# Optimization experiments

Hardware: AMD Instinct MI355X
Metric: run time of the kernel (lower is better)

Reference implementation:

```python
import math
import jax
import jax.numpy as jnp
import numpy as np
from jax import lax

HEADS = 4
TOPK = 8


def _gelu(x):
    return jax.nn.gelu(x, approximate=False)


def _ln(x, g, b, eps=1e-5):
    m = x.mean(-1, keepdims=True)
    v = ((x - m) ** 2).mean(-1, keepdims=True)
    return (x - m) * lax.rsqrt(v + eps) * g + b


def setup_inputs() -> dict:
    key = jax.random.key(0)
    ks = jax.random.split(key, 16)
    B, T, N, C, A = 16, 16, 196, 768, 192

    def w(k, shape, s=0.02):
        return jax.random.normal(k, shape, jnp.float32) * s

    return dict(
        x=w(ks[0], (B, T, N + 1, C), 1.0),
        down_w=w(ks[1], (A, C)), down_b=jnp.zeros((A,), jnp.float32),
        ldw_w=w(ks[2], (A, 1, 3, 3), 0.1),
        lpw_w=w(ks[3], (A, A), 0.05),
        lnorm_g=jnp.ones((A,), jnp.float32), lnorm_b=jnp.zeros((A,), jnp.float32),
        tdw_w=w(ks[4], (A, 1, 3), 0.1),
        tpw_w=w(ks[5], (A, A), 0.05),
        tmlp_w1=w(ks[6], (2 * A, A), 0.05), tmlp_b1=jnp.zeros((2 * A,), jnp.float32),
        tmlp_w2=w(ks[7], (A, 2 * A), 0.05), tmlp_b2=jnp.zeros((A,), jnp.float32),
        tnorm_g=jnp.ones((A,), jnp.float32), tnorm_b=jnp.zeros((A,), jnp.float32),
        attn_in_w=w(ks[8], (3 * A, A), 0.05), attn_in_b=jnp.zeros((3 * A,), jnp.float32),
        attn_out_w=w(ks[9], (A, A), 0.05), attn_out_b=jnp.zeros((A,), jnp.float32),
        aproj_w=w(ks[10], (A, A), 0.05), aproj_b=jnp.zeros((A,), jnp.float32),
        anorm_g=jnp.ones((A,), jnp.float32), anorm_b=jnp.zeros((A,), jnp.float32),
        gate_w1=w(ks[11], (A, 2 * A), 0.05), gate_b1=jnp.zeros((A,), jnp.float32),
        gate_w2=w(ks[12], (3 * A, A), 0.05), gate_b2=jnp.zeros((3 * A,), jnp.float32),
        up_w=w(ks[13], (C, A), 0.02), up_b=jnp.zeros((C,), jnp.float32),
        cls_w=w(ks[14], (C, A), 0.02), cls_b=jnp.zeros((C,), jnp.float32),
    )


def reference(x, down_w, down_b, ldw_w, lpw_w, lnorm_g, lnorm_b, tdw_w, tpw_w,
              tmlp_w1, tmlp_b1, tmlp_w2, tmlp_b2, tnorm_g, tnorm_b,
              attn_in_w, attn_in_b, attn_out_w, attn_out_b, aproj_w, aproj_b,
              anorm_g, anorm_b, gate_w1, gate_b1, gate_w2, gate_b2,
              up_w, up_b, cls_w, cls_b):
    cls_tok = x[:, :, :1, :]
    patch = x[:, :, 1:, :]
    b, t, n, _ = patch.shape
    hw = int(math.isqrt(n))
    a = down_w.shape[0]

    # down projection: [b,t,n,C] -> [b,t,n,A]
    ph = jnp.einsum('btnc,ac->btna', patch, down_w) + down_b
    # temporal difference, delta[:,0]=0
    delta = jnp.concatenate([jnp.zeros_like(ph[:, :1]), ph[:, 1:] - ph[:, :-1]], axis=1)

    # --- local path: depthwise 3x3 -> GELU -> pointwise 1x1 -> LN ---
    loc = ph.reshape(b * t, hw, hw, a).transpose(0, 3, 1, 2)  # (bt) a h w
    loc = lax.conv_general_dilated(loc, ldw_w, (1, 1), 'SAME',
                                   feature_group_count=a,
                                   dimension_numbers=('NCHW', 'OIHW', 'NCHW'))
    loc = _gelu(loc)
    loc = jnp.einsum('bchw,dc->bdhw', loc, lpw_w)
    loc = loc.transpose(0, 2, 3, 1).reshape(b, t, n, a)
    local = _ln(loc, lnorm_g, lnorm_b)

    # --- transition path: depthwise temporal conv -> GELU -> pointwise -> MLP -> LN ---
    tr = delta.transpose(0, 2, 3, 1).reshape(b * n, a, t)  # (bn) a t
    tr = lax.conv_general_dilated(tr, tdw_w, (1,), 'SAME',
                                  feature_group_count=a,
                                  dimension_numbers=('NCH', 'OIH', 'NCH'))
    tr = _gelu(tr)
    tr = jnp.einsum('nct,dc->ndt', tr, tpw_w)
    tr = tr.reshape(b, n, a, t).transpose(0, 3, 1, 2)  # b t n a
    h1 = _gelu(jnp.einsum('btna,ha->btnh', tr, tmlp_w1) + tmlp_b1)
    tr = jnp.einsum('btnh,ah->btna', h1, tmlp_w2) + tmlp_b2
    transition = _ln(tr, tnorm_g, tnorm_b)

    # --- relation anchor path: topk gather -> temporal MHA -> scatter_add -> LN ---
    kk = min(TOPK, n)
    sal = jnp.abs(delta).mean(-1)  # b t n
    _, idx = lax.top_k(sal, kk)    # b t k
    bi = jnp.arange(b)[:, None, None]
    ti = jnp.arange(t)[None, :, None]
    anchor = (ph + delta)[bi, ti, idx]  # b t k a
    tok = anchor.transpose(0, 2, 1, 3).reshape(b * kk, t, a)  # (bk) t a
    qkv = tok @ attn_in_w.T + attn_in_b
    q, k_, v = jnp.split(qkv, 3, axis=-1)
    dh = a // HEADS

    def heads(z):
        return z.reshape(b * kk, t, HEADS, dh).transpose(0, 2, 1, 3)

    q, k_, v = heads(q), heads(k_), heads(v)
    att = jax.nn.softmax(jnp.einsum('bhqd,bhkd->bhqk', q, k_) / math.sqrt(dh), axis=-1)
    out = jnp.einsum('bhqk,bhkd->bhqd', att, v).transpose(0, 2, 1, 3).reshape(b * kk, t, a)
    out = out @ attn_out_w.T + attn_out_b
    out = out @ aproj_w.T + aproj_b
    anchor_tok = out.reshape(b, kk, t, a).transpose(0, 2, 1, 3)  # b t k a
    anchor_map = jnp.zeros_like(ph).at[bi, ti, idx].add(anchor_tok)
    anchor_map = _ln(anchor_map, anorm_g, anorm_b)

    # --- softmax-gated 3-way fusion ---
    dp = jnp.abs(delta).mean((1, 2))      # b a
    ap = anchor_tok.mean((1, 2))          # b a
    g = jnp.concatenate([dp, ap], axis=-1)
    g = _gelu(g @ gate_w1.T + gate_b1) @ gate_w2.T + gate_b2
    gw = jax.nn.softmax(g.reshape(b, 3, a), axis=1)[:, :, None, None, :]
    fused = gw[:, 0] * local + gw[:, 1] * transition + gw[:, 2] * anchor_map

    patch_out = patch + fused @ up_w.T + up_b
    cls_out = cls_tok + fused.mean(2, keepdims=True) @ cls_w.T + cls_b
    return jnp.concatenate([cls_out, patch_out], axis=2)
```

## Files before the change

### kernel.cpp

```cpp
#include <hip/hip_runtime.h>
#include <math.h>

constexpr int Bb  = 16;
constexpr int Tt  = 16;
constexpr int Nn  = 196;
constexpr int Cc  = 768;
constexpr int Aa  = 192;
constexpr int KK  = 8;
constexpr int NCAND = 16;
constexpr int BT  = Bb * Tt;
constexpr int BTN = BT * Nn;
constexpr int BKT = Bb * KK * Tt;
constexpr size_t SZ = (size_t)BTN * Aa;

typedef unsigned short ushortt;
typedef __attribute__((ext_vector_type(8))) short bf16x8;
typedef __attribute__((ext_vector_type(4))) float f32x4;
typedef __attribute__((ext_vector_type(4))) unsigned short u16x4;
typedef __attribute__((ext_vector_type(8))) unsigned short u16x8;

static __device__ __forceinline__ float gelu_f(float x) {
  return 0.5f * x * (1.0f + erff(x * 0.7071067811865476f));
}
static __device__ __forceinline__ ushortt f2bf(float f) {
  unsigned u = __float_as_uint(f);
  u += 0x7FFFu + ((u >> 16) & 1u);
  return (ushortt)(u >> 16);
}
static __device__ __forceinline__ float bf2f(ushortt u) {
  return __uint_as_float(((unsigned)u) << 16);
}

template <typename AT, typename CT, int ROWMAP, int BIAS, int EPI>
__global__ __launch_bounds__(256) void gemm_mfma(
    const AT* __restrict__ Ain, const float* __restrict__ W,
    const float* __restrict__ bias, CT* __restrict__ Cout,
    const float* __restrict__ resid, int M, int Nc, int K) {
  constexpr int PIT = 40;
  __shared__ ushortt As[2][128 * PIT];
  __shared__ ushortt Bs[2][64 * PIT];
  const int tid = threadIdx.x;

  const int ncb = gridDim.x;
  const int nwg = ncb * gridDim.y;
  const int bid = blockIdx.y * ncb + blockIdx.x;
  const int cpx = nwg >> 3;
  const int swz = (bid & 7) * cpx + (bid >> 3);
  const int row0 = (swz / ncb) * 128;
  const int col0 = (swz % ncb) * 64;

  const int wid = tid >> 6;
  const int lane = tid & 63;
  const int wr = wid >> 1;
  const int wc = wid & 1;
  const int l15 = lane & 15;
  const int kgrp = lane >> 4;

  const int nsteps = K >> 5;

  const float* arowf[4];
  const ushortt* arowb[2];
  if constexpr (sizeof(AT) == 4) {
    const int quad = tid & 7, srow = tid >> 3;
#pragma unroll
    for (int p = 0; p < 4; ++p) {
      int r = row0 + srow + 32 * p;
      if (ROWMAP) {
        int bt = r / Nn;
        int n = r - bt * Nn;
        arowf[p] = (const float*)Ain + (size_t)(bt * (Nn + 1) + 1 + n) * K;
      } else {
        arowf[p] = (const float*)Ain + (size_t)r * K;
      }
    }
    (void)quad;
  } else {
    const int srow2 = tid >> 2;
#pragma unroll
    for (int p = 0; p < 2; ++p)
      arowb[p] = (const ushortt*)Ain + (size_t)(row0 + srow2 + 64 * p) * K;
  }
  const float* browp[2];
  {
    const int srow = tid >> 3;
#pragma unroll
    for (int p = 0; p < 2; ++p)
      browp[p] = W + (size_t)(col0 + srow + 32 * p) * K;
  }

  f32x4 acc[4][2];
#pragma unroll
  for (int i = 0; i < 4; ++i)
#pragma unroll
    for (int j = 0; j < 2; ++j) acc[i][j] = (f32x4){0.f, 0.f, 0.f, 0.f};

  float4 apre[4], bpre[2];
  u16x8 apreb[2];

#define STAGE_LOAD(k0)                                                       \
  if constexpr (sizeof(AT) == 4) {                                           \
    const int quad = tid & 7;                                                \
    _Pragma("unroll") for (int p = 0; p < 4; ++p)                            \
        apre[p] = *(const float4*)(arowf[p] + (k0) + quad * 4);              \
  } else {                                                                   \
    const int quad2 = tid & 3;                                               \
    _Pragma("unroll") for (int p = 0; p < 2; ++p)                            \
        apreb[p] = *(const u16x8*)(arowb[p] + (k0) + quad2 * 8);             \
  }                                                                          \
  {                                                                          \
    const int quad = tid & 7;                                                \
    _Pragma("unroll") for (int p = 0; p < 2; ++p)                            \
        bpre[p] = *(const float4*)(browp[p] + (k0) + quad * 4);              \
  }

#define STAGE_WRITE(buf)                                                     \
  if constexpr (sizeof(AT) == 4) {                                           \
    const int quad = tid & 7, srow = tid >> 3;                               \
    _Pragma("unroll") for (int p = 0; p < 4; ++p) {                          \
      u16x4 b = {f2bf(apre[p].x), f2bf(apre[p].y), f2bf(apre[p].z),          \
                 f2bf(apre[p].w)};                                           \
      *(u16x4*)&As[buf][(srow + 32 * p) * PIT + quad * 4] = b;               \
    }                                                                        \
  } else {                                                                   \
    const int quad2 = tid & 3, srow2 = tid >> 2;                             \
    _Pragma("unroll") for (int p = 0; p < 2; ++p)                            \
        *(u16x8*)&As[buf][(srow2 + 64 * p) * PIT + quad2 * 8] = apreb[p];    \
  }                                                                          \
  {                                                                          \
    const int quad = tid & 7, srow = tid >> 3;                               \
    _Pragma("unroll") for (int p = 0; p < 2; ++p) {                          \
      u16x4 b = {f2bf(bpre[p].x), f2bf(bpre[p].y), f2bf(bpre[p].z),          \
                 f2bf(bpre[p].w)};                                           \
      *(u16x4*)&Bs[buf][(srow + 32 * p) * PIT + quad * 4] = b;               \
    }                                                                        \
  }

  STAGE_LOAD(0);
  STAGE_WRITE(0);
  __syncthreads();

  int cur = 0;
  for (int step = 0; step < nsteps; ++step) {
    const bool pref = (step + 1 < nsteps);
    if (pref) {
      int k0 = (step + 1) << 5;
      STAGE_LOAD(k0);
    }
    bf16x8 af[4], bfv[2];
#pragma unroll
    for (int fm = 0; fm < 4; ++fm)
      af[fm] = *(const bf16x8*)&As[cur][(wr * 64 + fm * 16 + l15) * PIT + kgrp * 8];
#pragma unroll
    for (int fn = 0; fn < 2; ++fn)
      bfv[fn] = *(const bf16x8*)&Bs[cur][(wc * 32 + fn * 16 + l15) * PIT + kgrp * 8];
#pragma unroll
    for (int fm = 0; fm < 4; ++fm)
#pragma unroll
      for (int fn = 0; fn < 2; ++fn)
        acc[fm][fn] = __builtin_amdgcn_mfma_f32_16x16x32_bf16(
            af[fm], bfv[fn], acc[fm][fn], 0, 0, 0);
    if (pref) {
      STAGE_WRITE(cur ^ 1);
    }
    __syncthreads();
    cur ^= 1;
  }
#undef STAGE_LOAD
#undef STAGE_WRITE

#pragma unroll
  for (int fm = 0; fm < 4; ++fm) {
    int rbase = row0 + wr * 64 + fm * 16 + kgrp * 4;
#pragma unroll
    for (int fn = 0; fn < 2; ++fn) {
      int c = col0 + wc * 32 + fn * 16 + l15;
      float bv = BIAS ? bias[c] : 0.f;
#pragma unroll
      for (int j = 0; j < 4; ++j) {
        int r = rbase + j;
        float v = acc[fm][fn][j] + bv;
        if (EPI == 1) v = gelu_f(v);
        if (EPI == 2) {
          int bt = r / Nn;
          int n = r - bt * Nn;
          size_t off = (size_t)(bt * (Nn + 1) + 1 + n) * Nc + c;
          ((float*)Cout)[off] = resid[off] + v;
        } else {
          if constexpr (sizeof(CT) == 4)
            Cout[(size_t)r * Nc + c] = (CT)v;
          else
            ((ushortt*)Cout)[(size_t)r * Nc + c] = f2bf(v);
        }
      }
    }
  }
}

__global__ void delta_kernel(const float* __restrict__ ph,
                             float* __restrict__ delta,
                             float* __restrict__ dppart) {
  int bt = blockIdx.x;
  int t = bt & 15;
  int a = threadIdx.x;
  const float* cur = ph + (size_t)bt * Nn * Aa + a;
  float* dl = delta + (size_t)bt * Nn * Aa + a;
  float acc = 0.f;
  if (t == 0) {
    for (int n = 0; n < Nn; ++n) dl[(size_t)n * Aa] = 0.f;
  } else {
    const float* prev = cur - (size_t)Nn * Aa;
    for (int n = 0; n < Nn; ++n) {
      float d = cur[(size_t)n * Aa] - prev[(size_t)n * Aa];
      dl[(size_t)n * Aa] = d;
      acc += fabsf(d);
    }
  }
  dppart[bt * Aa + a] = acc;
}

__global__ void sal_kernel(const float* __restrict__ delta,
                           float* __restrict__ sal) {
  int row = blockIdx.x * 4 + (threadIdx.x >> 6);
  int lane = threadIdx.x & 63;
  const float* d = delta + (size_t)row * Aa;
  float s = fabsf(d[lane]) + fabsf(d[lane + 64]) + fabsf(d[lane + 128]);
#pragma unroll
  for (int off = 32; off > 0; off >>= 1) s += __shfl_xor(s, off, 64);
  if (lane == 0) sal[row] = s * (1.0f / 192.0f);
}

__global__ void topcand_kernel(const float* __restrict__ sal,
                               int* __restrict__ cand) {
  int bt = blockIdx.x;
  int lane = threadIdx.x;
  unsigned long long key[4];
#pragma unroll
  for (int j = 0; j < 4; ++j) {
    int n = lane + 64 * j;
    if (n < Nn) {
      unsigned fb = __float_as_uint(sal[(size_t)bt * Nn + n]);
      key[j] = ((unsigned long long)fb << 32) |
               (unsigned long long)(0xFFFFFFFFu - (unsigned)n);
    } else {
      key[j] = 0ULL;
    }
  }
  for (int r = 0; r < NCAND; ++r) {
    unsigned long long m = key[0];
    if (key[1] > m) m = key[1];
    if (key[2] > m) m = key[2];
    if (key[3] > m) m = key[3];
#pragma unroll
    for (int off = 32; off > 0; off >>= 1) {
      unsigned long long o = __shfl_xor(m, off, 64);
      if (o > m) m = o;
    }
    if (lane == 0)
      cand[bt * NCAND + r] = (int)(0xFFFFFFFFu - (unsigned)(m & 0xFFFFFFFFull));
#pragma unroll
    for (int j = 0; j < 4; ++j)
      if (key[j] == m) key[j] = 0ULL;
  }
}

__global__ __launch_bounds__(192) void refine_kernel(
    const float* __restrict__ x, const float* __restrict__ down_w,
    const int* __restrict__ cand, double* __restrict__ sal64) {
  int bt = blockIdx.x;
  int grp = blockIdx.y;
  int t = bt & 15;
  int a = threadIdx.x;
  if (t == 0) {
    if (a < 8) sal64[bt * NCAND + grp * 8 + a] = 0.0;
    return;
  }
  __shared__ double sdiff[8][Cc];
  __shared__ double sabs[8][Aa];
  const float* xt = x + (size_t)bt * (Nn + 1) * Cc;
  const float* xp = xt - (size_t)(Nn + 1) * Cc;
  for (int g = 0; g < 8; ++g) {
    int n = cand[bt * NCAND + grp * 8 + g];
    const float* rt = xt + (size_t)(1 + n) * Cc;
    const float* rp = xp + (size_t)(1 + n) * Cc;
    for (int c = a; c < Cc; c += 192)
      sdiff[g][c] = (double)rt[c] - (double)rp[c];
  }
  __syncthreads();
  double acc[8] = {};
  const float* wrow = down_w + (size_t)a * Cc;
  for (int c0 = 0; c0 < Cc; c0 += 4) {
    float4 w4 = *(const float4*)(wrow + c0);
#pragma unroll
    for (int g = 0; g < 8; ++g) {
      acc[g] += (double)w4.x * sdiff[g][c0] + (double)w4.y * sdiff[g][c0 + 1] +
                (double)w4.z * sdiff[g][c0 + 2] +
                (double)w4.w * sdiff[g][c0 + 3];
    }
  }
#pragma unroll
  for (int g = 0; g < 8; ++g) sabs[g][a] = fabs(acc[g]);
  __syncthreads();
  if (a < 8) {
    double s = 0.0;
    for (int i = 0; i < Aa; ++i) s += sabs[a][i];
    sal64[bt * NCAND + grp * 8 + a] = s * (1.0 / 192.0);
  }
}

__global__ void select_kernel(const double* __restrict__ sal64,
                              const int* __restrict__ cand,
                              int* __restrict__ idx) {
  int bt = blockIdx.x;
  int t = bt & 15;
  if (threadIdx.x != 0) return;
  if (t == 0) {
    for (int r = 0; r < KK; ++r) idx[bt * KK + r] = r;
    return;
  }
  double v[NCAND];
  int nn[NCAND];
  bool used[NCAND];
  for (int i = 0; i < NCAND; ++i) {
    v[i] = sal64[bt * NCAND + i];
    nn[i] = cand[bt * NCAND + i];
    used[i] = false;
  }
  for (int r = 0; r < KK; ++r) {
    int best = -1;
    for (int i = 0; i < NCAND; ++i) {
      if (used[i]) continue;
      if (best < 0 || v[i] > v[best] ||
          (v[i] == v[best] && nn[i] < nn[best]))
        best = i;
    }
    used[best] = true;
    idx[bt * KK + r] = nn[best];
  }
}

__global__ void gather_kernel(const float* __restrict__ ph,
                              const float* __restrict__ delta,
                              const int* __restrict__ idx,
                              float* __restrict__ tok) {
  int row = blockIdx.x;
  int t = row & 15;
  int bk = row >> 4;
  int b = bk >> 3, k = bk & 7;
  int a = threadIdx.x;
  int n = idx[(b * 16 + t) * KK + k];
  size_t off = ((size_t)(b * 16 + t) * Nn + n) * Aa + a;
  tok[(size_t)row * Aa + a] = ph[off] + delta[off];
}

__global__ __launch_bounds__(256) void attn_core(
    const float* __restrict__ qkv, float* __restrict__ o) {
  constexpr int P = 580;
  __shared__ float sq[16 * P];
  __shared__ float ssc[4][16][17];
  int bk = blockIdx.x;
  int tid = threadIdx.x;
  const float* src = qkv + (size_t)bk * 16 * 576;
  for (int e = tid; e < 16 * 144; e += 256) {
    int r = e / 144, c4 = e % 144;
    float4 v = *(const float4*)(src + r * 576 + c4 * 4);
    *(float4*)(&sq[r * P + c4 * 4]) = v;
  }
  __syncthreads();
  int h = tid >> 6, lane = tid & 63;
#pragma unroll
  for (int s4 = 0; s4 < 4; ++s4) {
    int e = lane + 64 * s4;
    int i = e >> 4, j = e & 15;
    const float* q = sq + i * P + h * 48;
    const float* k2 = sq + j * P + 192 + h * 48;
    float s = 0.f;
#pragma unroll
    for (int d = 0; d < 48; ++d) s = fmaf(q[d], k2[d], s);
    ssc[h][i][j] = s * 0.14433756729740643f;
  }
  __syncthreads();
  if (lane < 16) {
    float* r = ssc[h][lane];
    float mx = r[0];
    for (int j = 1; j < 16; ++j) mx = fmaxf(mx, r[j]);
    float sum = 0.f;
    for (int j = 0; j < 16; ++j) {
      float ev = expf(r[j] - mx);
      r[j] = ev;
      sum += ev;
    }
    float inv = 1.0f / sum;
    for (int j = 0; j < 16; ++j) r[j] *= inv;
  }
  __syncthreads();
#pragma unroll
  for (int s4 = 0; s4 < 12; ++s4) {
    int e = lane + 64 * s4;
    int i = e / 48, d = e - i * 48;
    float s = 0.f;
#pragma unroll
    for (int j = 0; j < 16; ++j)
      s = fmaf(ssc[h][i][j], sq[j * P + 384 + h * 48 + d], s);
    o[((size_t)bk * 16 + i) * 192 + h * 48 + d] = s;
  }
}

__global__ void appart_kernel(const float* __restrict__ attout,
                              float* __restrict__ appart) {
  int bk = blockIdx.x;
  int a = threadIdx.x;
  float s = 0.f;
  for (int t = 0; t < Tt; ++t)
    s += attout[((size_t)bk * Tt + t) * Aa + a];
  appart[bk * Aa + a] = s;
}

__global__ void conv2d_kernel(const float* __restrict__ ph,
                              const float* __restrict__ ldw,
                              ushortt* __restrict__ og) {
  size_t e = (size_t)blockIdx.x * 256 + threadIdx.x;
  int a = (int)(e % Aa);
  size_t r = e / Aa;
  int n = (int)(r % Nn);
  int bt = (int)(r / Nn);
  int y = n / 14, x = n % 14;
  const float* base = ph + (size_t)bt * Nn * Aa + a;
  const float* w = ldw + a * 9;
  float s = 0.f;
#pragma unroll
  for (int dy = -1; dy <= 1; ++dy) {
    int yy = y + dy;
    if (yy < 0 || yy >= 14) continue;
#pragma unroll
    for (int dx = -1; dx <= 1; ++dx) {
      int xc = x + dx;
      if (xc < 0 || xc >= 14) continue;
      s = fmaf(base[(size_t)(yy * 14 + xc) * Aa], w[(dy + 1) * 3 + (dx + 1)], s);
    }
  }
  og[e] = f2bf(gelu_f(s));
}

__global__ void conv1d_kernel(const float* __restrict__ delta,
                              const float* __restrict__ tdw,
                              ushortt* __restrict__ og) {
  size_t e = (size_t)blockIdx.x * 256 + threadIdx.x;
  int a = (int)(e % Aa);
  size_t r = e / Aa;
  int n = (int)(r % Nn);
  int bt = (int)(r / Nn);
  int t = bt & 15, b = bt >> 4;
  const float* w = tdw + a * 3;
  float s = 0.f;
#pragma unroll
  for (int j = 0; j < 3; ++j) {
    int tt = t + j - 1;
    if (tt >= 0 && tt < Tt)
      s = fmaf(delta[((size_t)(b * Tt + tt) * Nn + n) * Aa + a], w[j], s);
  }
  og[e] = f2bf(gelu_f(s));
}

template <typename T>
__global__ void ln_kernel(T* __restrict__ buf, const float* __restrict__ g,
                          const float* __restrict__ bb) {
  size_t row = (size_t)blockIdx.x * 4 + (threadIdx.x >> 6);
  int lane = threadIdx.x & 63;
  T* p = buf + row * Aa;
  float v0, v1, v2;
  if constexpr (sizeof(T) == 4) {
    v0 = p[lane]; v1 = p[lane + 64]; v2 = p[lane + 128];
  } else {
    v0 = bf2f(p[lane]); v1 = bf2f(p[lane + 64]); v2 = bf2f(p[lane + 128]);
  }
  float s = v0 + v1 + v2;
#pragma unroll
  for (int off = 32; off > 0; off >>= 1) s += __shfl_xor(s, off, 64);
  float m = s * (1.0f / 192.0f);
  float d0 = v0 - m, d1 = v1 - m, d2 = v2 - m;
  float ss = d0 * d0 + d1 * d1 + d2 * d2;
#pragma unroll
  for (int off = 32; off > 0; off >>= 1) ss += __shfl_xor(ss, off, 64);
  float inv = rsqrtf(ss * (1.0f / 192.0f) + 1e-5f);
  float o0 = d0 * inv * g[lane] + bb[lane];
  float o1 = d1 * inv * g[lane + 64] + bb[lane + 64];
  float o2 = d2 * inv * g[lane + 128] + bb[lane + 128];
  if constexpr (sizeof(T) == 4) {
    p[lane] = o0; p[lane + 64] = o1; p[lane + 128] = o2;
  } else {
    p[lane] = f2bf(o0); p[lane + 64] = f2bf(o1); p[lane + 128] = f2bf(o2);
  }
}

__global__ void scatter_kernel(const float* __restrict__ attout,
                               const int* __restrict__ idx,
                               ushortt* __restrict__ amap) {
  int bt = blockIdx.x;
  int b = bt >> 4, t = bt & 15;
  for (int e = threadIdx.x; e < KK * Aa; e += 256) {
    int k = e / Aa, a = e % Aa;
    int n = idx[bt * KK + k];
    amap[((size_t)bt * Nn + n) * Aa + a] =
        f2bf(attout[((size_t)(b * KK + k) * Tt + t) * Aa + a]);
  }
}

__global__ void gate_kernel(const float* __restrict__ dppart,
                            const float* __restrict__ appart,
                            const float* __restrict__ w1,
                            const float* __restrict__ b1,
                            const float* __restrict__ w2,
                            const float* __restrict__ b2,
                            float* __restrict__ gw) {
  int b = blockIdx.x;
  __shared__ float sg[2 * Aa];
  __shared__ float sh[Aa];
  int tid = threadIdx.x;
  {
    float d = 0.f;
    for (int t2 = 0; t2 < Tt; ++t2) d += dppart[(b * Tt + t2) * Aa + tid];
    sg[tid] = d * (1.0f / 3136.0f);
    float a = 0.f;
    for (int k2 = 0; k2 < KK; ++k2) a += appart[(b * KK + k2) * Aa + tid];
    sg[Aa + tid] = a * (1.0f / 128.0f);
  }
  __syncthreads();
  {
    const float* w = w1 + (size_t)tid * 2 * Aa;
    float s = b1[tid];
#pragma unroll 8
    for (int j = 0; j < 2 * Aa; ++j) s = fmaf(sg[j], w[j], s);
    sh[tid] = gelu_f(s);
  }
  __syncthreads();
  float v[3];
#pragma unroll
  for (int i = 0; i < 3; ++i) {
    const float* w = w2 + (size_t)(i * Aa + tid) * Aa;
    float s = b2[i * Aa + tid];
#pragma unroll 8
    for (int j = 0; j < Aa; ++j) s = fmaf(sh[j], w[j], s);
    v[i] = s;
  }
  float mx = fmaxf(v[0], fmaxf(v[1], v[2]));
  float e0 = expf(v[0] - mx), e1 = expf(v[1] - mx), e2 = expf(v[2] - mx);
  float inv = 1.0f / (e0 + e1 + e2);
  gw[(b * 3 + 0) * Aa + tid] = e0 * inv;
  gw[(b * 3 + 1) * Aa + tid] = e1 * inv;
  gw[(b * 3 + 2) * Aa + tid] = e2 * inv;
}

__global__ void fused_kernel(const ushortt* __restrict__ local,
                             const ushortt* __restrict__ trans,
                             const ushortt* __restrict__ amap,
                             const float* __restrict__ gw,
                             ushortt* __restrict__ fused,
                             float* __restrict__ fmean) {
  int bt = blockIdx.x;
  int b = bt >> 4;
  int a = threadIdx.x;
  float g0 = gw[(b * 3 + 0) * Aa + a];
  float g1 = gw[(b * 3 + 1) * Aa + a];
  float g2 = gw[(b * 3 + 2) * Aa + a];
  size_t base = (size_t)bt * Nn * Aa + a;
  float acc = 0.f;
  for (int n = 0; n < Nn; ++n) {
    size_t o = base + (size_t)n * Aa;
    float f = g0 * bf2f(local[o]) + g1 * bf2f(trans[o]) + g2 * bf2f(amap[o]);
    fused[o] = f2bf(f);
    acc += f;
  }
  fmean[bt * Aa + a] = acc;
}

__global__ void cls_kernel(const float* __restrict__ fmean,
                           const float* __restrict__ cw,
                           const float* __restrict__ cb,
                           const float* __restrict__ x,
                           float* __restrict__ out) {
  int bt = blockIdx.x;
  __shared__ float fm[Aa];
  int tid = threadIdx.x;
  if (tid < Aa) fm[tid] = fmean[bt * Aa + tid] * (1.0f / 196.0f);
  __syncthreads();
  for (int c = tid; c < Cc; c += 256) {
    const float* w = cw + (size_t)c * Aa;
    float s = cb[c];
#pragma unroll 8
    for (int a = 0; a < Aa; ++a) s = fmaf(fm[a], w[a], s);
    size_t off = (size_t)bt * (Nn + 1) * Cc + c;
    out[off] = x[off] + s;
  }
}

extern "C" void kernel_launch(void* const* d_in, const int* in_sizes, int n_in,
                              void* d_out, int out_size, void* d_ws,
                              size_t ws_size, hipStream_t stream) {
  const float* x = (const float*)d_in[0];
  const float* down_w = (const float*)d_in[1];
  const float* down_b = (const float*)d_in[2];
  const float* ldw_w = (const float*)d_in[3];
  const float* lpw_w = (const float*)d_in[4];
  const float* lnorm_g = (const float*)d_in[5];
  const float* lnorm_b = (const float*)d_in[6];
  const float* tdw_w = (const float*)d_in[7];
  const float* tpw_w = (const float*)d_in[8];
  const float* tmlp_w1 = (const float*)d_in[9];
  const float* tmlp_b1 = (const float*)d_in[10];
  const float* tmlp_w2 = (const float*)d_in[11];
  const float* tmlp_b2 = (const float*)d_in[12];
  const float* tnorm_g = (const float*)d_in[13];
  const float* tnorm_b = (const float*)d_in[14];
  const float* attn_in_w = (const float*)d_in[15];
  const float* attn_in_b = (const float*)d_in[16];
  const float* attn_out_w = (const float*)d_in[17];
  const float* attn_out_b = (const float*)d_in[18];
  const float* aproj_w = (const float*)d_in[19];
  const float* aproj_b = (const float*)d_in[20];
  const float* anorm_g = (const float*)d_in[21];
  const float* anorm_b = (const float*)d_in[22];
  const float* gate_w1 = (const float*)d_in[23];
  const float* gate_b1 = (const float*)d_in[24];
  const float* gate_w2 = (const float*)d_in[25];
  const float* gate_b2 = (const float*)d_in[26];
  const float* up_w = (const float*)d_in[27];
  const float* up_b = (const float*)d_in[28];
  const float* cls_w = (const float*)d_in[29];
  const float* cls_b = (const float*)d_in[30];
  float* out = (float*)d_out;

  float* ws = (float*)d_ws;
  float* W0 = ws;
  float* W1 = W0 + SZ;
  float* W2 = W1 + SZ;
  float* W3 = W2 + 2 * SZ;
  float* sal = W3 + SZ;
  float* attout = sal + BTN;
  float* dppart = attout + (size_t)BKT * Aa;
  float* appart = dppart + (size_t)BT * Aa;
  float* gw = appart + (size_t)Bb * KK * Aa;
  float* fmean = gw + (size_t)Bb * 3 * Aa;
  double* sal64 = (double*)(fmean + (size_t)BT * Aa);
  int* cand = (int*)(sal64 + (size_t)BT * NCAND);
  int* idx = cand + (size_t)BT * NCAND;

  ushortt* trp_b   = (ushortt*)W0;
  ushortt* amap_b  = (ushortt*)W0;
  ushortt* trans_b = (ushortt*)W1;
  ushortt* locg_b  = (ushortt*)W2;
  ushortt* trg_b   = (ushortt*)W2;
  ushortt* h1_b    = (ushortt*)W2;
  ushortt* fused_b = (ushortt*)W2;
  ushortt* local_b = (ushortt*)W3;

  float* tok   = W2;
  float* qkvb  = tok + (size_t)BKT * Aa;
  float* obuf  = qkvb + (size_t)BKT * 3 * Aa;
  float* proj1 = obuf + (size_t)BKT * Aa;

  gemm_mfma<float, float, 1, 1, 0><<<dim3(3, 392), 256, 0, stream>>>(
      x, down_w, down_b, W0, nullptr, BTN, Aa, Cc);
  delta_kernel<<<BT, Aa, 0, stream>>>(W0, W1, dppart);
  sal_kernel<<<BTN / 4, 256, 0, stream>>>(W1, sal);
  topcand_kernel<<<BT, 64, 0, stream>>>(sal, cand);
  refine_kernel<<<dim3(BT, 2), 192, 0, stream>>>(x, down_w, cand, sal64);
  select_kernel<<<BT, 64, 0, stream>>>(sal64, cand, idx);
  gather_kernel<<<BKT, Aa, 0, stream>>>(W0, W1, idx, tok);
  gemm_mfma<float, float, 0, 1, 0><<<dim3(9, 16), 256, 0, stream>>>(
      tok, attn_in_w, attn_in_b, qkvb, nullptr, BKT, 3 * Aa, Aa);
  attn_core<<<Bb * KK, 256, 0, stream>>>(qkvb, obuf);
  gemm_mfma<float, float, 0, 1, 0><<<dim3(3, 16), 256, 0, stream>>>(
      obuf, attn_out_w, attn_out_b, proj1, nullptr, BKT, Aa, Aa);
  gemm_mfma<float, float, 0, 1, 0><<<dim3(3, 16), 256, 0, stream>>>(
      proj1, aproj_w, aproj_b, attout, nullptr, BKT, Aa, Aa);
  appart_kernel<<<Bb * KK, Aa, 0, stream>>>(attout, appart);
  conv2d_kernel<<<(unsigned)(SZ / 256), 256, 0, stream>>>(W0, ldw_w, locg_b);
  gemm_mfma<ushortt, ushortt, 0, 0, 0><<<dim3(3, 392), 256, 0, stream>>>(
      locg_b, lpw_w, nullptr, local_b, nullptr, BTN, Aa, Aa);
  ln_kernel<ushortt><<<BTN / 4, 256, 0, stream>>>(local_b, lnorm_g, lnorm_b);
  conv1d_kernel<<<(unsigned)(SZ / 256), 256, 0, stream>>>(W1, tdw_w, trg_b);
  gemm_mfma<ushortt, ushortt, 0, 0, 0><<<dim3(3, 392), 256, 0, stream>>>(
      trg_b, tpw_w, nullptr, trp_b, nullptr, BTN, Aa, Aa);
  gemm_mfma<ushortt, ushortt, 0, 1, 1><<<dim3(6, 392), 256, 0, stream>>>(
      trp_b, tmlp_w1, tmlp_b1, h1_b, nullptr, BTN, 2 * Aa, Aa);
  gemm_mfma<ushortt, ushortt, 0, 1, 0><<<dim3(3, 392), 256, 0, stream>>>(
      h1_b, tmlp_w2, tmlp_b2, trans_b, nullptr, BTN, Aa, 2 * Aa);
  ln_kernel<ushortt><<<BTN / 4, 256, 0, stream>>>(trans_b, tnorm_g, tnorm_b);
  hipMemsetAsync(amap_b, 0, SZ * sizeof(ushortt), stream);
  scatter_kernel<<<BT, 256, 0, stream>>>(attout, idx, amap_b);
  ln_kernel<ushortt><<<BTN / 4, 256, 0, stream>>>(amap_b, anorm_g, anorm_b);
  gate_kernel<<<Bb, Aa, 0, stream>>>(dppart, appart, gate_w1, gate_b1,
                                     gate_w2, gate_b2, gw);
  fused_kernel<<<BT, Aa, 0, stream>>>(local_b, trans_b, amap_b, gw, fused_b,
                                      fmean);
  gemm_mfma<ushortt, float, 0, 1, 2><<<dim3(12, 392), 256, 0, stream>>>(
      fused_b, up_w, up_b, out, x, BTN, Cc, Aa);
  cls_kernel<<<BT, 256, 0, stream>>>(fmean, cls_w, cls_b, x, out);
}
```

Before: 648.1 us.

## Store ph/delta/tokens in bf16, widen GEMM N-tile to 96, parallelize refine

```diff
diff --git a/kernel.cpp b/kernel.cpp
--- a/kernel.cpp
+++ b/kernel.cpp
@@ -38,7 +38,7 @@
     const float* __restrict__ resid, int M, int Nc, int K) {
   constexpr int PIT = 40;
   __shared__ ushortt As[2][128 * PIT];
-  __shared__ ushortt Bs[2][64 * PIT];
+  __shared__ ushortt Bs[2][96 * PIT];
   const int tid = threadIdx.x;
 
   const int ncb = gridDim.x;
@@ -47,7 +47,7 @@
   const int cpx = nwg >> 3;
   const int swz = (bid & 7) * cpx + (bid >> 3);
   const int row0 = (swz / ncb) * 128;
-  const int col0 = (swz % ncb) * 64;
+  const int col0 = (swz % ncb) * 96;
 
   const int wid = tid >> 6;
   const int lane = tid & 63;
@@ -61,7 +61,7 @@
   const float* arowf[4];
   const ushortt* arowb[2];
   if constexpr (sizeof(AT) == 4) {
-    const int quad = tid & 7, srow = tid >> 3;
+    const int srow = tid >> 3;
 #pragma unroll
     for (int p = 0; p < 4; ++p) {
       int r = row0 + srow + 32 * p;
@@ -73,28 +73,27 @@
         arowf[p] = (const float*)Ain + (size_t)r * K;
       }
     }
-    (void)quad;
   } else {
     const int srow2 = tid >> 2;
 #pragma unroll
     for (int p = 0; p < 2; ++p)
       arowb[p] = (const ushortt*)Ain + (size_t)(row0 + srow2 + 64 * p) * K;
   }
-  const float* browp[2];
+  const float* browp[3];
   {
     const int srow = tid >> 3;
 #pragma unroll
-    for (int p = 0; p < 2; ++p)
+    for (int p = 0; p < 3; ++p)
       browp[p] = W + (size_t)(col0 + srow + 32 * p) * K;
   }
 
-  f32x4 acc[4][2];
+  f32x4 acc[4][3];
 #pragma unroll
   for (int i = 0; i < 4; ++i)
 #pragma unroll
-    for (int j = 0; j < 2; ++j) acc[i][j] = (f32x4){0.f, 0.f, 0.f, 0.f};
-
-  float4 apre[4], bpre[2];
+    for (int j = 0; j < 3; ++j) acc[i][j] = (f32x4){0.f, 0.f, 0.f, 0.f};
+
+  float4 apre[4], bpre[3];
   u16x8 apreb[2];
 
 #define STAGE_LOAD(k0)                                                       \
@@ -109,7 +108,7 @@
   }                                                                          \
   {                                                                          \
     const int quad = tid & 7;                                                \
-    _Pragma("unroll") for (int p = 0; p < 2; ++p)                            \
+    _Pragma("unroll") for (int p = 0; p < 3; ++p)                            \
         bpre[p] = *(const float4*)(browp[p] + (k0) + quad * 4);              \
   }
 
@@ -128,7 +127,7 @@
   }                                                                          \
   {                                                                          \
     const int quad = tid & 7, srow = tid >> 3;                               \
-    _Pragma("unroll") for (int p = 0; p < 2; ++p) {                          \
+    _Pragma("unroll") for (int p = 0; p < 3; ++p) {                          \
       u16x4 b = {f2bf(bpre[p].x), f2bf(bpre[p].y), f2bf(bpre[p].z),          \
                  f2bf(bpre[p].w)};                                           \
       *(u16x4*)&Bs[buf][(srow + 32 * p) * PIT + quad * 4] = b;               \
@@ -146,17 +145,17 @@
       int k0 = (step + 1) << 5;
       STAGE_LOAD(k0);
     }
-    bf16x8 af[4], bfv[2];
+    bf16x8 af[4], bfv[3];
 #pragma unroll
     for (int fm = 0; fm < 4; ++fm)
       af[fm] = *(const bf16x8*)&As[cur][(wr * 64 + fm * 16 + l15) * PIT + kgrp * 8];
 #pragma unroll
-    for (int fn = 0; fn < 2; ++fn)
-      bfv[fn] = *(const bf16x8*)&Bs[cur][(wc * 32 + fn * 16 + l15) * PIT + kgrp * 8];
+    for (int fn = 0; fn < 3; ++fn)
+      bfv[fn] = *(const bf16x8*)&Bs[cur][(wc * 48 + fn * 16 + l15) * PIT + kgrp * 8];
 #pragma unroll
     for (int fm = 0; fm < 4; ++fm)
 #pragma unroll
-      for (int fn = 0; fn < 2; ++fn)
+      for (int fn = 0; fn < 3; ++fn)
         acc[fm][fn] = __builtin_amdgcn_mfma_f32_16x16x32_bf16(
             af[fm], bfv[fn], acc[fm][fn], 0, 0, 0);
     if (pref) {
@@ -172,8 +171,8 @@
   for (int fm = 0; fm < 4; ++fm) {
     int rbase = row0 + wr * 64 + fm * 16 + kgrp * 4;
 #pragma unroll
-    for (int fn = 0; fn < 2; ++fn) {
-      int c = col0 + wc * 32 + fn * 16 + l15;
+    for (int fn = 0; fn < 3; ++fn) {
+      int c = col0 + wc * 48 + fn * 16 + l15;
       float bv = BIAS ? bias[c] : 0.f;
 #pragma unroll
       for (int j = 0; j < 4; ++j) {
@@ -196,34 +195,35 @@
   }
 }
 
-__global__ void delta_kernel(const float* __restrict__ ph,
-                             float* __restrict__ delta,
+__global__ void delta_kernel(const ushortt* __restrict__ ph,
+                             ushortt* __restrict__ delta,
                              float* __restrict__ dppart) {
   int bt = blockIdx.x;
   int t = bt & 15;
   int a = threadIdx.x;
-  const float* cur = ph + (size_t)bt * Nn * Aa + a;
-  float* dl = delta + (size_t)bt * Nn * Aa + a;
+  const ushortt* cur = ph + (size_t)bt * Nn * Aa + a;
+  ushortt* dl = delta + (size_t)bt * Nn * Aa + a;
   float acc = 0.f;
   if (t == 0) {
-    for (int n = 0; n < Nn; ++n) dl[(size_t)n * Aa] = 0.f;
+    for (int n = 0; n < Nn; ++n) dl[(size_t)n * Aa] = 0;
   } else {
-    const float* prev = cur - (size_t)Nn * Aa;
+    const ushortt* prev = cur - (size_t)Nn * Aa;
     for (int n = 0; n < Nn; ++n) {
-      float d = cur[(size_t)n * Aa] - prev[(size_t)n * Aa];
-      dl[(size_t)n * Aa] = d;
+      float d = bf2f(cur[(size_t)n * Aa]) - bf2f(prev[(size_t)n * Aa]);
+      dl[(size_t)n * Aa] = f2bf(d);
       acc += fabsf(d);
     }
   }
   dppart[bt * Aa + a] = acc;
 }
 
-__global__ void sal_kernel(const float* __restrict__ delta,
+__global__ void sal_kernel(const ushortt* __restrict__ delta,
                            float* __restrict__ sal) {
   int row = blockIdx.x * 4 + (threadIdx.x >> 6);
   int lane = threadIdx.x & 63;
-  const float* d = delta + (size_t)row * Aa;
-  float s = fabsf(d[lane]) + fabsf(d[lane + 64]) + fabsf(d[lane + 128]);
+  const ushortt* d = delta + (size_t)row * Aa;
+  float s = fabsf(bf2f(d[lane])) + fabsf(bf2f(d[lane + 64])) +
+            fabsf(bf2f(d[lane + 128]));
 #pragma unroll
   for (int off = 32; off > 0; off >>= 1) s += __shfl_xor(s, off, 64);
   if (lane == 0) sal[row] = s * (1.0f / 192.0f);
@@ -267,44 +267,36 @@
     const float* __restrict__ x, const float* __restrict__ down_w,
     const int* __restrict__ cand, double* __restrict__ sal64) {
   int bt = blockIdx.x;
-  int grp = blockIdx.y;
+  int ci = blockIdx.y;
   int t = bt & 15;
-  int a = threadIdx.x;
+  int tid = threadIdx.x;
   if (t == 0) {
-    if (a < 8) sal64[bt * NCAND + grp * 8 + a] = 0.0;
+    if (tid == 0) sal64[bt * NCAND + ci] = 0.0;
     return;
   }
-  __shared__ double sdiff[8][Cc];
-  __shared__ double sabs[8][Aa];
-  const float* xt = x + (size_t)bt * (Nn + 1) * Cc;
-  const float* xp = xt - (size_t)(Nn + 1) * Cc;
-  for (int g = 0; g < 8; ++g) {
-    int n = cand[bt * NCAND + grp * 8 + g];
-    const float* rt = xt + (size_t)(1 + n) * Cc;
-    const float* rp = xp + (size_t)(1 + n) * Cc;
-    for (int c = a; c < Cc; c += 192)
-      sdiff[g][c] = (double)rt[c] - (double)rp[c];
-  }
-  __syncthreads();
-  double acc[8] = {};
-  const float* wrow = down_w + (size_t)a * Cc;
-  for (int c0 = 0; c0 < Cc; c0 += 4) {
-    float4 w4 = *(const float4*)(wrow + c0);
-#pragma unroll
-    for (int g = 0; g < 8; ++g) {
-      acc[g] += (double)w4.x * sdiff[g][c0] + (double)w4.y * sdiff[g][c0 + 1] +
-                (double)w4.z * sdiff[g][c0 + 2] +
-                (double)w4.w * sdiff[g][c0 + 3];
-    }
-  }
-#pragma unroll
-  for (int g = 0; g < 8; ++g) sabs[g][a] = fabs(acc[g]);
-  __syncthreads();
-  if (a < 8) {
-    double s = 0.0;
-    for (int i = 0; i < Aa; ++i) s += sabs[a][i];
-    sal64[bt * NCAND + grp * 8 + a] = s * (1.0 / 192.0);
-  }
+  int n = cand[bt * NCAND + ci];
+  const float* rt = x + ((size_t)bt * (Nn + 1) + 1 + n) * Cc;
+  const float* rp = rt - (size_t)(Nn + 1) * Cc;
+  const float* wrow = down_w + (size_t)tid * Cc;
+  double acc = 0.0;
+  for (int c = 0; c < Cc; c += 4) {
+    float4 w4 = *(const float4*)(wrow + c);
+    float4 a4 = *(const float4*)(rt + c);
+    float4 b4 = *(const float4*)(rp + c);
+    acc += (double)w4.x * ((double)a4.x - (double)b4.x) +
+           (double)w4.y * ((double)a4.y - (double)b4.y) +
+           (double)w4.z * ((double)a4.z - (double)b4.z) +
+           (double)w4.w * ((double)a4.w - (double)b4.w);
+  }
+  double v = fabs(acc);
+#pragma unroll
+  for (int off = 32; off > 0; off >>= 1) v += __shfl_xor(v, off, 64);
+  __shared__ double part[3];
+  int wv = tid >> 6, ln = tid & 63;
+  if (ln == 0) part[wv] = v;
+  __syncthreads();
+  if (tid == 0)
+    sal64[bt * NCAND + ci] = (part[0] + part[1] + part[2]) * (1.0 / 192.0);
 }
 
 __global__ void select_kernel(const double* __restrict__ sal64,
@@ -338,10 +330,10 @@
   }
 }
 
-__global__ void gather_kernel(const float* __restrict__ ph,
-                              const float* __restrict__ delta,
+__global__ void gather_kernel(const ushortt* __restrict__ ph,
+                              const ushortt* __restrict__ delta,
                               const int* __restrict__ idx,
-                              float* __restrict__ tok) {
+                              ushortt* __restrict__ tok) {
   int row = blockIdx.x;
   int t = row & 15;
   int bk = row >> 4;
@@ -349,7 +341,7 @@
   int a = threadIdx.x;
   int n = idx[(b * 16 + t) * KK + k];
   size_t off = ((size_t)(b * 16 + t) * Nn + n) * Aa + a;
-  tok[(size_t)row * Aa + a] = ph[off] + delta[off];
+  tok[(size_t)row * Aa + a] = f2bf(bf2f(ph[off]) + bf2f(delta[off]));
 }
 
 __global__ __launch_bounds__(256) void attn_core(
@@ -415,7 +407,7 @@
   appart[bk * Aa + a] = s;
 }
 
-__global__ void conv2d_kernel(const float* __restrict__ ph,
+__global__ void conv2d_kernel(const ushortt* __restrict__ ph,
                               const float* __restrict__ ldw,
                               ushortt* __restrict__ og) {
   size_t e = (size_t)blockIdx.x * 256 + threadIdx.x;
@@ -424,7 +416,7 @@
   int n = (int)(r % Nn);
   int bt = (int)(r / Nn);
   int y = n / 14, x = n % 14;
-  const float* base = ph + (size_t)bt * Nn * Aa + a;
+  const ushortt* base = ph + (size_t)bt * Nn * Aa + a;
   const float* w = ldw + a * 9;
   float s = 0.f;
 #pragma unroll
@@ -435,13 +427,14 @@
     for (int dx = -1; dx <= 1; ++dx) {
       int xc = x + dx;
       if (xc < 0 || xc >= 14) continue;
-      s = fmaf(base[(size_t)(yy * 14 + xc) * Aa], w[(dy + 1) * 3 + (dx + 1)], s);
+      s = fmaf(bf2f(base[(size_t)(yy * 14 + xc) * Aa]),
+               w[(dy + 1) * 3 + (dx + 1)], s);
     }
   }
   og[e] = f2bf(gelu_f(s));
 }
 
-__global__ void conv1d_kernel(const float* __restrict__ delta,
+__global__ void conv1d_kernel(const ushortt* __restrict__ delta,
                               const float* __restrict__ tdw,
                               ushortt* __restrict__ og) {
   size_t e = (size_t)blockIdx.x * 256 + threadIdx.x;
@@ -456,23 +449,18 @@
   for (int j = 0; j < 3; ++j) {
     int tt = t + j - 1;
     if (tt >= 0 && tt < Tt)
-      s = fmaf(delta[((size_t)(b * Tt + tt) * Nn + n) * Aa + a], w[j], s);
+      s = fmaf(bf2f(delta[((size_t)(b * Tt + tt) * Nn + n) * Aa + a]), w[j], s);
   }
   og[e] = f2bf(gelu_f(s));
 }
 
-template <typename T>
-__global__ void ln_kernel(T* __restrict__ buf, const float* __restrict__ g,
+__global__ void ln_kernel(ushortt* __restrict__ buf,
+                          const float* __restrict__ g,
                           const float* __restrict__ bb) {
   size_t row = (size_t)blockIdx.x * 4 + (threadIdx.x >> 6);
   int lane = threadIdx.x & 63;
-  T* p = buf + row * Aa;
-  float v0, v1, v2;
-  if constexpr (sizeof(T) == 4) {
-    v0 = p[lane]; v1 = p[lane + 64]; v2 = p[lane + 128];
-  } else {
-    v0 = bf2f(p[lane]); v1 = bf2f(p[lane + 64]); v2 = bf2f(p[lane + 128]);
-  }
+  ushortt* p = buf + row * Aa;
+  float v0 = bf2f(p[lane]), v1 = bf2f(p[lane + 64]), v2 = bf2f(p[lane + 128]);
   float s = v0 + v1 + v2;
 #pragma unroll
   for (int off = 32; off > 0; off >>= 1) s += __shfl_xor(s, off, 64);
@@ -482,14 +470,9 @@
 #pragma unroll
   for (int off = 32; off > 0; off >>= 1) ss += __shfl_xor(ss, off, 64);
   float inv = rsqrtf(ss * (1.0f / 192.0f) + 1e-5f);
-  float o0 = d0 * inv * g[lane] + bb[lane];
-  float o1 = d1 * inv * g[lane + 64] + bb[lane + 64];
-  float o2 = d2 * inv * g[lane + 128] + bb[lane + 128];
-  if constexpr (sizeof(T) == 4) {
-    p[lane] = o0; p[lane + 64] = o1; p[lane + 128] = o2;
-  } else {
-    p[lane] = f2bf(o0); p[lane + 64] = f2bf(o1); p[lane + 128] = f2bf(o2);
-  }
+  p[lane] = f2bf(d0 * inv * g[lane] + bb[lane]);
+  p[lane + 64] = f2bf(d1 * inv * g[lane + 64] + bb[lane + 64]);
+  p[lane + 128] = f2bf(d2 * inv * g[lane + 128] + bb[lane + 128]);
 }
 
 __global__ void scatter_kernel(const float* __restrict__ attout,
@@ -644,8 +627,10 @@
   int* cand = (int*)(sal64 + (size_t)BT * NCAND);
   int* idx = cand + (size_t)BT * NCAND;
 
+  ushortt* ph_b    = (ushortt*)W0;
   ushortt* trp_b   = (ushortt*)W0;
   ushortt* amap_b  = (ushortt*)W0;
+  ushortt* delta_b = (ushortt*)W1;
   ushortt* trans_b = (ushortt*)W1;
   ushortt* locg_b  = (ushortt*)W2;
   ushortt* trg_b   = (ushortt*)W2;
@@ -653,47 +638,47 @@
   ushortt* fused_b = (ushortt*)W2;
   ushortt* local_b = (ushortt*)W3;
 
-  float* tok   = W2;
-  float* qkvb  = tok + (size_t)BKT * Aa;
+  ushortt* tok_b = (ushortt*)W2;
+  float* qkvb  = W2 + (size_t)BKT * Aa / 2;
   float* obuf  = qkvb + (size_t)BKT * 3 * Aa;
   float* proj1 = obuf + (size_t)BKT * Aa;
 
-  gemm_mfma<float, float, 1, 1, 0><<<dim3(3, 392), 256, 0, stream>>>(
-      x, down_w, down_b, W0, nullptr, BTN, Aa, Cc);
-  delta_kernel<<<BT, Aa, 0, stream>>>(W0, W1, dppart);
-  sal_kernel<<<BTN / 4, 256, 0, stream>>>(W1, sal);
+  gemm_mfma<float, ushortt, 1, 1, 0><<<dim3(2, 392), 256, 0, stream>>>(
+      x, down_w, down_b, ph_b, nullptr, BTN, Aa, Cc);
+  delta_kernel<<<BT, Aa, 0, stream>>>(ph_b, delta_b, dppart);
+  sal_kernel<<<BTN / 4, 256, 0, stream>>>(delta_b, sal);
   topcand_kernel<<<BT, 64, 0, stream>>>(sal, cand);
-  refine_kernel<<<dim3(BT, 2), 192, 0, stream>>>(x, down_w, cand, sal64);
+  refine_kernel<<<dim3(BT, NCAND), 192, 0, stream>>>(x, down_w, cand, sal64);
   select_kernel<<<BT, 64, 0, stream>>>(sal64, cand, idx);
-  gather_kernel<<<BKT, Aa, 0, stream>>>(W0, W1, idx, tok);
-  gemm_mfma<float, float, 0, 1, 0><<<dim3(9, 16), 256, 0, stream>>>(
-      tok, attn_in_w, attn_in_b, qkvb, nullptr, BKT, 3 * Aa, Aa);
+  gather_kernel<<<BKT, Aa, 0, stream>>>(ph_b, delta_b, idx, tok_b);
+  gemm_mfma<ushortt, float, 0, 1, 0><<<dim3(6, 16), 256, 0, stream>>>(
+      tok_b, attn_in_w, attn_in_b, qkvb, nullptr, BKT, 3 * Aa, Aa);
   attn_core<<<Bb * KK, 256, 0, stream>>>(qkvb, obuf);
-  gemm_mfma<float, float, 0, 1, 0><<<dim3(3, 16), 256, 0, stream>>>(
+  gemm_mfma<float, float, 0, 1, 0><<<dim3(2, 16), 256, 0, stream>>>(
       obuf, attn_out_w, attn_out_b, proj1, nullptr, BKT, Aa, Aa);
-  gemm_mfma<float, float, 0, 1, 0><<<dim3(3, 16), 256, 0, stream>>>(
+  gemm_mfma<float, float, 0, 1, 0><<<dim3(2, 16), 256, 0, stream>>>(
       proj1, aproj_w, aproj_b, attout, nullptr, BKT, Aa, Aa);
   appart_kernel<<<Bb * KK, Aa, 0, stream>>>(attout, appart);
-  conv2d_kernel<<<(unsigned)(SZ / 256), 256, 0, stream>>>(W0, ldw_w, locg_b);
-  gemm_mfma<ushortt, ushortt, 0, 0, 0><<<dim3(3, 392), 256, 0, stream>>>(
+  conv2d_kernel<<<(unsigned)(SZ / 256), 256, 0, stream>>>(ph_b, ldw_w, locg_b);
+  gemm_mfma<ushortt, ushortt, 0, 0, 0><<<dim3(2, 392), 256, 0, stream>>>(
       locg_b, lpw_w, nullptr, local_b, nullptr, BTN, Aa, Aa);
-  ln_kernel<ushortt><<<BTN / 4, 256, 0, stream>>>(local_b, lnorm_g, lnorm_b);
-  conv1d_kernel<<<(unsigned)(SZ / 256), 256, 0, stream>>>(W1, tdw_w, trg_b);
-  gemm_mfma<ushortt, ushortt, 0, 0, 0><<<dim3(3, 392), 256, 0, stream>>>(
+  ln_kernel<<<BTN / 4, 256, 0, stream>>>(local_b, lnorm_g, lnorm_b);
+  conv1d_kernel<<<(unsigned)(SZ / 256), 256, 0, stream>>>(delta_b, tdw_w, trg_b);
+  gemm_mfma<ushortt, ushortt, 0, 0, 0><<<dim3(2, 392), 256, 0, stream>>>(
       trg_b, tpw_w, nullptr, trp_b, nullptr, BTN, Aa, Aa);
-  gemm_mfma<ushortt, ushortt, 0, 1, 1><<<dim3(6, 392), 256, 0, stream>>>(
+  gemm_mfma<ushortt, ushortt, 0, 1, 1><<<dim3(4, 392), 256, 0, stream>>>(
       trp_b, tmlp_w1, tmlp_b1, h1_b, nullptr, BTN, 2 * Aa, Aa);
-  gemm_mfma<ushortt, ushortt, 0, 1, 0><<<dim3(3, 392), 256, 0, stream>>>(
+  gemm_mfma<ushortt, ushortt, 0, 1, 0><<<dim3(2, 392), 256, 0, stream>>>(
       h1_b, tmlp_w2, tmlp_b2, trans_b, nullptr, BTN, Aa, 2 * Aa);
-  ln_kernel<ushortt><<<BTN / 4, 256, 0, stream>>>(trans_b, tnorm_g, tnorm_b);
+  ln_kernel<<<BTN / 4, 256, 0, stream>>>(trans_b, tnorm_g, tnorm_b);
   hipMemsetAsync(amap_b, 0, SZ * sizeof(ushortt), stream);
   scatter_kernel<<<BT, 256, 0, stream>>>(attout, idx, amap_b);
-  ln_kernel<ushortt><<<BTN / 4, 256, 0, stream>>>(amap_b, anorm_g, anorm_b);
+  ln_kernel<<<BTN / 4, 256, 0, stream>>>(amap_b, anorm_g, anorm_b);
   gate_kernel<<<Bb, Aa, 0, stream>>>(dppart, appart, gate_w1, gate_b1,
                                      gate_w2, gate_b2, gw);
   fused_kernel<<<BT, Aa, 0, stream>>>(local_b, trans_b, amap_b, gw, fused_b,
                                       fmean);
-  gemm_mfma<ushortt, float, 0, 1, 2><<<dim3(12, 392), 256, 0, stream>>>(
+  gemm_mfma<ushortt, float, 0, 1, 2><<<dim3(8, 392), 256, 0, stream>>>(
       fused_b, up_w, up_b, out, x, BTN, Cc, Aa);
   cls_kernel<<<BT, 256, 0, stream>>>(fmean, cls_w, cls_b, x, out);
 }
```

Result: slower. 1.019 ms (+57.2%).
